# Kernel optimization log

Hardware: AMD Instinct MI355X
Metric: run time of the kernel (lower is better)

The kernel has to match this reference:

```python
import jax, jax.numpy as jnp
import numpy as np

B, S, V, E, HL = 64, 30, 5000, 300, 256
TWOH = 2 * HL
KB, MAPD, MEMD, MLP, NCLS = 512, 512, 512, 1024, 32
L, T, NMOD, NOPS = 8, 9, 9, 6
IH, IW, CIN = 15, 10, 512 + 128


def setup_inputs():
    key = jax.random.key(0)
    ks = iter(jax.random.split(key, 64))
    g = lambda shape, s=0.05: jax.random.normal(next(ks), shape, jnp.float32) * s
    inp = {}
    inp['image'] = g((B, CIN, IH, IW), 1.0)
    inp['ques'] = jax.random.randint(next(ks), (B, S), 0, V)
    ql = jnp.sort(jax.random.randint(next(ks), (B,), 1, S + 1))[::-1]
    inp['q_len'] = ql.at[0].set(S)
    inp['embed_W'] = g((V, E))
    for d in ('f', 'b'):
        inp['lstm_Wi_' + d] = g((E, 4 * HL))
        inp['lstm_Wh_' + d] = g((HL, 4 * HL))
        inp['lstm_b_' + d] = jnp.zeros((4 * HL,), jnp.float32)
    inp['W1'] = g((T, TWOH, TWOH))
    inp['b_1'] = jnp.zeros((TWOH,), jnp.float32)
    inp['W2_w'] = g((2 * TWOH, TWOH)); inp['W2_b'] = jnp.zeros((TWOH,), jnp.float32)
    inp['W3'] = g((TWOH,))
    inp['c_0'] = g((TWOH,), 1.0)
    inp['Wmod'] = g((TWOH, NMOD))
    inp['ic1_w'] = g((KB, CIN)); inp['ic1_b'] = g((KB,), 1.0)
    inp['ic2_w'] = g((KB, KB)); inp['ic2_b'] = g((KB,), 1.0)
    inp['i2m_w'] = g((MAPD, KB)); inp['i2m_b'] = g((MAPD,), 1.0)
    inp['t2m_w'] = g((TWOH, MAPD)); inp['t2m_b'] = jnp.zeros((MAPD,), jnp.float32)
    inp['cell3_ow'] = g((4, NOPS), 1.0)
    inp['cell3_cw'] = g((4, MAPD)); inp['cell3_cb'] = jnp.zeros((4,), jnp.float32)
    inp['cell4_ow'] = g((2, NOPS), 1.0)
    inp['cell4_cw'] = g((2, MAPD)); inp['cell4_cb'] = jnp.zeros((2,), jnp.float32)
    inp['ans_ow'] = g((2, NOPS), 1.0)
    inp['ans_W'] = g((2, 2 * MAPD, MEMD)); inp['ans_b'] = jnp.zeros((2, MEMD), jnp.float32)
    inp['out1_w'] = g((TWOH + MEMD, MLP)); inp['out1_b'] = jnp.zeros((MLP,), jnp.float32)
    inp['out2_w'] = g((MLP, NCLS)); inp['out2_b'] = jnp.zeros((NCLS,), jnp.float32)
    return inp


def _conv1x1(x, w, b):
    return jnp.einsum('bchw,oc->bohw', x, w) + b[None, :, None, None]


def _lstm_dir(xW, Wh, mask, reverse):
    # xW: [S,B,4H], mask: [S,B,1] ; torch LSTM gate order i,f,g,o
    Bn, Hn = xW.shape[1], Wh.shape[0]
    def step(carry, inp):
        h, c = carry
        xw, m = inp
        z = xw + h @ Wh
        i, f, gg, o = jnp.split(z, 4, axis=-1)
        cn = jax.nn.sigmoid(f) * c + jax.nn.sigmoid(i) * jnp.tanh(gg)
        hn = jax.nn.sigmoid(o) * jnp.tanh(cn)
        return (jnp.where(m, hn, h), jnp.where(m, cn, c)), jnp.where(m, hn, 0.0)
    init = (jnp.zeros((Bn, Hn), xW.dtype), jnp.zeros((Bn, Hn), xW.dtype))
    (hF, _), outs = jax.lax.scan(step, init, (xW, mask), reverse=reverse)
    return hF, outs


def _mix3(ow, x, a, t):
    # soft op mixing (DARTS-style) for 3-input cells: x [B,D,H,W], a [B,H,W], t [B,D]
    w = jax.nn.softmax(ow)
    a4 = a[:, None]; t4 = t[:, :, None, None]
    ops = (x * t4, x + t4, x * a4, x * t4 * a4, x, a4 * t4)
    return jax.nn.elu(sum(w[k] * ops[k] for k in range(NOPS)))


def _mix4(ow, x, a1, a2, t):
    w = jax.nn.softmax(ow)
    a14 = a1[:, None]; a24 = a2[:, None]; t4 = t[:, :, None, None]
    ops = (x * t4, x + t4, x * a14, x * a24, x * a14 * a24, x * t4 * (a14 + a24))
    return jax.nn.elu(sum(w[k] * ops[k] for k in range(NOPS)))


def _forward(image, ques, q_len, embed_W, lstm_Wi_f, lstm_Wh_f, lstm_b_f, lstm_Wi_b, lstm_Wh_b, lstm_b_b, W1, b_1, W2_w, W2_b, W3, c_0, Wmod, ic1_w, ic1_b, ic2_w, ic2_b, i2m_w, i2m_b, t2m_w, t2m_b, cell3_ow, cell3_cw, cell3_cb, cell4_ow, cell4_cw, cell4_cb, ans_ow, ans_W, ans_b, out1_w, out1_b, out2_w, out2_b):
    # img_conv (1x1 conv -> ELU -> 1x1 conv)
    x = jax.nn.elu(_conv1x1(image, ic1_w, ic1_b))
    x = _conv1x1(x, ic2_w, ic2_b)
    Bn, _, Hh, Ww = x.shape
    Sn = ques.shape[1]
    # bi-LSTM over the (packed, i.e. masked) question
    emb = embed_W[ques]                                   # [B,S,E]
    mask = (jnp.arange(Sn)[None, :] < q_len[:, None])     # [B,S]
    mT = mask.T[:, :, None].astype(x.dtype) > 0           # [S,B,1] bool
    xWf = (emb @ lstm_Wi_f + lstm_b_f).transpose(1, 0, 2)
    xWb = (emb @ lstm_Wi_b + lstm_b_b).transpose(1, 0, 2)
    hF, oF = _lstm_dir(xWf, lstm_Wh_f, mT, False)
    hB, oB = _lstm_dir(xWb, lstm_Wh_b, mT, True)
    lstm_out = jnp.concatenate([oF, oB], -1).transpose(1, 0, 2)  # [B,S,2H], zero at pads
    q = jnp.concatenate([hF, hB], -1)                            # [B,2H]
    img_map = _conv1x1(x, i2m_w, i2m_b)                          # [B,MAP,H,W]
    stack = jnp.zeros((Bn, Hh, Ww, L), x.dtype)
    p = jnp.zeros((Bn, L), x.dtype).at[:, 0].set(1.0)
    mem = jnp.zeros((Bn, MEMD), x.dtype)
    c_prev = jnp.tile(c_0[None], (Bn, 1))
    e0 = jnp.zeros((L,), x.dtype).at[0].set(1.0)
    imp_loss = jnp.float32(0.0)
    read = lambda st, pp: jnp.einsum('bhwl,bl->bhw', st, pp)
    dec = lambda pp: jnp.concatenate([pp[:, 1:], jnp.zeros_like(pp[:, :1])], 1) + pp * e0
    for t in range(T):
        u = jnp.concatenate([q @ W1[t] + b_1, c_prev], 1) @ W2_w + W2_b  # [B,2H]
        wl = u @ Wmod                                                     # [B,9]
        ls = jax.nn.log_softmax(wl, axis=1)
        imp_loss = imp_loss - jnp.sum(jnp.exp(ls) * ls)
        w = jnp.exp(ls)
        attn = jax.nn.softmax(jnp.einsum('bsh,h->bs', lstm_out * u[:, None, :], W3), axis=1)
        c = jnp.einsum('bs,bsh->bh', attn, lstm_out)
        c_prev = c
        tmap = c @ t2m_w + t2m_b
        stacks, ps = [], []
        a_top = read(stack, p)     # attention at stack top
        # modules 0-3: overwrite at current pointer (pointer shift is commented out in source)
        for m in range(4):
            out = jnp.einsum('bdhw,d->bhw', _mix3(cell3_ow[m], img_map, a_top, tmap), cell3_cw[m]) + cell3_cb[m]
            pb = p[:, None, None, :]
            stacks.append(stack * (1.0 - pb) + out[..., None] * pb)
            ps.append(p)
        # modules 4-5: pop one (soft pointer decrement), then write
        p_dec = dec(p)
        a2 = read(stack, p_dec)
        for m in range(2):
            out = jnp.einsum('bdhw,d->bhw', _mix4(cell4_ow[m], img_map, a_top, a2, tmap), cell4_cw[m]) + cell4_cb[m]
            pb = p_dec[:, None, None, :]
            stacks.append(stack * (1.0 - pb) + out[..., None] * pb)
            ps.append(p_dec)
        # modules 6-7: answer cells -> memory update, stack untouched
        pooled6 = jnp.mean(_mix3(ans_ow[0], img_map, a_top, tmap), axis=(2, 3))
        mem6 = jnp.concatenate([pooled6, tmap], 1) @ ans_W[0] + ans_b[0]
        stacks.append(stack); ps.append(p)
        pooled7 = jnp.mean(_mix4(ans_ow[1], img_map, a_top, a2, tmap), axis=(2, 3))
        mem7 = jnp.concatenate([pooled7, tmap], 1) @ ans_W[1] + ans_b[1]
        stacks.append(stack); ps.append(p_dec)
        # module 8: NoOp
        stacks.append(stack); ps.append(p)
        # soft mixing over modules (the scatter-heavy part)
        stack = jnp.einsum('bm,bmhwl->bhwl', w, jnp.stack(stacks, 1))
        p = jnp.einsum('bm,bml->bl', w, jnp.stack(ps, 1))
        mem = w[:, 6:7] * mem6 + w[:, 7:8] * mem7 + (1.0 - w[:, 6:7] - w[:, 7:8]) * mem
    h1 = jax.nn.elu(jnp.concatenate([q, mem], 1) @ out1_w + out1_b)
    logits = h1 @ out2_w + out2_b
    return logits, imp_loss


def reference(image, ques, q_len, embed_W, lstm_Wi_f, lstm_Wh_f, lstm_b_f, lstm_Wi_b, lstm_Wh_b, lstm_b_b, W1, b_1, W2_w, W2_b, W3, c_0, Wmod, ic1_w, ic1_b, ic2_w, ic2_b, i2m_w, i2m_b, t2m_w, t2m_b, cell3_ow, cell3_cw, cell3_cb, cell4_ow, cell4_cw, cell4_cb, ans_ow, ans_W, ans_b, out1_w, out1_b, out2_w, out2_b):
    return _forward(image, ques, q_len, embed_W, lstm_Wi_f, lstm_Wh_f, lstm_b_f, lstm_Wi_b, lstm_Wh_b, lstm_b_b, W1, b_1, W2_w, W2_b, W3, c_0, Wmod, ic1_w, ic1_b, ic2_w, ic2_b, i2m_w, i2m_b, t2m_w, t2m_b, cell3_ow, cell3_cw, cell3_cb, cell4_ow, cell4_cw, cell4_cb, ans_ow, ans_W, ans_b, out1_w, out1_b, out2_w, out2_b)
```

## Files before the change

kernel.cpp:

```cpp
#include <hip/hip_runtime.h>
#include <hip/hip_fp16.h>
#include <math.h>

#define DEV __device__ __forceinline__

DEV float fexp(float x){ return __expf(x); }
DEV float elu_(float x){ return x > 0.f ? x : fexp(x) - 1.f; }
DEV float sigm_(float x){ return 1.f/(1.f + fexp(-x)); }
DEV float tanh_(float x){ float e = fexp(2.f*x); return 1.f - 2.f/(e + 1.f); }
DEV unsigned bf16r(float x){ unsigned u = __float_as_uint(x);
  return (u + 0x7fffu + ((u>>16)&1u)) >> 16; }
DEV float blo(unsigned u){ return __uint_as_float(u << 16); }
DEV float bhi(unsigned u){ return __uint_as_float(u & 0xffff0000u); }
DEV float bl(unsigned short u){ return __uint_as_float(((unsigned)u) << 16); }

using frag  = __attribute__((ext_vector_type(8))) short;
using fragh = __attribute__((ext_vector_type(8))) _Float16;
using f32x4 = __attribute__((ext_vector_type(4))) float;

DEV uint4 cload16w(const void* p){
  uint4 r;
  asm volatile("global_load_dwordx4 %0, %1, off sc0 sc1\n\ts_waitcnt vmcnt(0)"
               : "=v"(r) : "v"(p) : "memory");
  return r;
// ... 171 lines not shown
    const short* bk = Bbase + (((size_t)kc*Ng) << 9);
    frag b0 = *(const frag*)(bk);
    frag b1 = *(const frag*)(bk + 512);
    frag b2 = *(const frag*)(bk + 1024);
    frag b3 = *(const frag*)(bk + 1536);
    acc0 = __builtin_amdgcn_mfma_f32_16x16x32_bf16(a, b0, acc0, 0, 0, 0);
    acc1 = __builtin_amdgcn_mfma_f32_16x16x32_bf16(a, b1, acc1, 0, 0, 0);
    acc2 = __builtin_amdgcn_mfma_f32_16x16x32_bf16(a, b2, acc2, 0, 0, 0);
    acc3 = __builtin_amdgcn_mfma_f32_16x16x32_bf16(a, b3, acc3, 0, 0, 0);
  }
  {
    int colb = lane & 15, rowb = (lane >> 4)*4;
#pragma unroll
    for (int r = 0; r < 4; ++r) {
      lds[w][rowb+r][ 0+colb] = acc0[r];
      lds[w][rowb+r][16+colb] = acc1[r];
      lds[w][rowb+r][32+colb] = acc2[r];
      lds[w][rowb+r][48+colb] = acc3[r];
    }
  }
  __syncthreads();
  if (mode == 0) {
    float* C = (float*)Cout;
    int mloc = lane >> 2, q4 = lane & 3;
    size_t rowoff = (size_t)(mt*16 + mloc)*N + ncol0 + q4*16;
#pragma unroll
    for (int i = 0; i < 4; ++i) {
      float4 v = *(float4*)&lds[w][mloc][q4*16 + i*4];
      const float* bp = bias + ncol0 + q4*16 + i*4;
      v.x += bp[0]; v.y += bp[1]; v.z += bp[2]; v.w += bp[3];
      if (act) { v.x = elu_(v.x); v.y = elu_(v.y); v.z = elu_(v.z); v.w = elu_(v.w); }
      *(float4*)&C[rowoff + i*4] = v;
    }
  } else if (mode == 1) {
    short* C = (short*)Cout;
    int m = lane & 15, qb = (lane >> 4)*8;
#pragma unroll
    for (int h = 0; h < 2; ++h) {
      int nl = h*32 + qb;
      unsigned o[4];
#pragma unroll
      for (int jj = 0; jj < 4; ++jj) {
        float v0 = lds[w][m][nl + 2*jj]     + bias[ncol0 + nl + 2*jj];
        float v1 = lds[w][m][nl + 2*jj + 1] + bias[ncol0 + nl + 2*jj + 1];
        if (act) { v0 = elu_(v0); v1 = elu_(v1); }
        o[jj] = bf16r(v0) | (bf16r(v1) << 16);
      }
      *(uint4*)(C + (((size_t)mt*KCout + (ncol0 >> 5) + h) << 9) + lane*8)
          = make_uint4(o[0], o[1], o[2], o[3]);
    }
  } else {
    unsigned short* C = (unsigned short*)Cout;
    int row = lane >> 2, cb = (lane & 3)*16;
#pragma unroll
    for (int h = 0; h < 2; ++h) {
      unsigned o[4];
#pragma unroll
      for (int jj = 0; jj < 4; ++jj) {
        float v0 = lds[w][row][cb + h*8 + 2*jj]     + bias[ncol0 + cb + h*8 + 2*jj];
        float v1 = lds[w][row][cb + h*8 + 2*jj + 1] + bias[ncol0 + cb + h*8 + 2*jj + 1];
        if (act) { v0 = elu_(v0); v1 = elu_(v1); }
        o[jj] = bf16r(v0) | (bf16r(v1) << 16);
      }
      *(uint4*)&C[(size_t)(mt*16 + row)*N + ncol0 + cb + h*8]
          = make_uint4(o[0], o[1], o[2], o[3]);
    }
  }
}

__global__ __launch_bounds__(512)
void gemm64b_k(const float* __restrict__ A1, long zA1, int K1log,
               const float* __restrict__ A2, int K2,
               const float* __restrict__ B, long zB,
               const float* __restrict__ bias, int zbias,
               float* __restrict__ C, long zC, int N, int act)
{
  const int K1 = 1 << K1log;
  const int Kt = K1 + K2;
  __shared__ __align__(16) float As[8][1024];
  __shared__ float part[8][8][64];
  const int tid = threadIdx.x;
  const int z = blockIdx.z;
  const int r0 = blockIdx.y*8;
  {
    const float* a1 = A1 + (size_t)z*zA1;
    const int nf4 = (8*K1) >> 2;
    for (int e4 = tid; e4 < nf4; e4 += 512) {
      int r = e4 >> (K1log-2);
      int k4 = (e4 & ((K1>>2)-1)) << 2;
      *(float4*)&As[r][k4] = *(const float4*)&a1[(size_t)(r0+r)*K1 + k4];
    }
    if (K2 > 0) {
      for (int e4 = tid; e4 < 1024; e4 += 512) {
        int r = e4 >> 7;
        int k4 = (e4 & 127) << 2;
        *(float4*)&As[r][K1+k4] = *(const float4*)&A2[(size_t)(r0+r)*512 + k4];
      }
    }
  }
  __syncthreads();
  const int lane = tid & 63, w = tid >> 6;
  const int n = blockIdx.x*64 + lane;
  const bool nv = n < N;
  const int kseg = Kt >> 3;
  const int k0 = w*kseg;
  const float* Bp = B + (size_t)z*zB + (size_t)k0*N + (nv ? n : 0);
  float acc[8] = {0,0,0,0,0,0,0,0};
#pragma unroll 8
  for (int kk = 0; kk < kseg; ++kk) {
    float bv = nv ? Bp[(size_t)kk*N] : 0.f;
    int k = k0 + kk;
#pragma unroll
    for (int r = 0; r < 8; ++r) acc[r] += As[r][k]*bv;
  }
#pragma unroll
  for (int r = 0; r < 8; ++r) part[w][r][lane] = acc[r];
  __syncthreads();
  {
    int r = tid >> 6, c = tid & 63;
    int nn = blockIdx.x*64 + c;
    if (nn < N) {
      float s = 0.f;
#pragma unroll
      for (int w2 = 0; w2 < 8; ++w2) s += part[w2][r][c];
      s += bias ? bias[(size_t)z*zbias + nn] : 0.f;
      if (act == 1) s = elu_(s);
      C[(size_t)z*zC + (size_t)(r0+r)*N + nn] = s;
    }
  }
}

__global__ __launch_bounds__(256)
void lstmc1_k(const float* __restrict__ xWf, const float* __restrict__ xWb,
              const unsigned* __restrict__ whT, const int* __restrict__ qlen,
              unsigned long long* __restrict__ hbuf, int* __restrict__ flags,
              float* __restrict__ lstm_out, float* __restrict__ qout,
              const short* __restrict__ c1Ap, const short* __restrict__ c1Bp,
              const float* __restrict__ c1bias, short* __restrict__ c1out)
{
  const int tid = threadIdx.x, lane = tid & 63, w = tid >> 6;
  __shared__ union {
    unsigned short Wl[65536];
    float lds[4][16][68];
  } sm;

  if (blockIdx.x >= 32) {
    const int bx2 = (int)blockIdx.x - 32;
    const int mt = (bx2 >> 3)*4 + w;
    const int ncol0 = (bx2 & 7)*64;
    const short* Abase = c1Ap + (((size_t)mt*20) << 9) + lane*8;
    const short* Bbase = c1Bp + (((size_t)(bx2 & 7)*4) << 9) + lane*8;
    f32x4 acc0 = {0.f,0.f,0.f,0.f}, acc1 = acc0, acc2 = acc0, acc3 = acc0;
#pragma unroll 2
    for (int kc = 0; kc < 20; ++kc) {
      frag a = *(const frag*)(Abase + ((size_t)kc << 9));
      const short* bk = Bbase + (((size_t)kc*32) << 9);
      frag b0 = *(const frag*)(bk);
      frag b1 = *(const frag*)(bk + 512);
      frag b2 = *(const frag*)(bk + 1024);
      frag b3 = *(const frag*)(bk + 1536);
      acc0 = __builtin_amdgcn_mfma_f32_16x16x32_bf16(a, b0, acc0, 0, 0, 0);
      acc1 = __builtin_amdgcn_mfma_f32_16x16x32_bf16(a, b1, acc1, 0, 0, 0);
      acc2 = __builtin_amdgcn_mfma_f32_16x16x32_bf16(a, b2, acc2, 0, 0, 0);
      acc3 = __builtin_amdgcn_mfma_f32_16x16x32_bf16(a, b3, acc3, 0, 0, 0);
    }
    {
      int colb = lane & 15, rowb = (lane >> 4)*4;
#pragma unroll
      for (int r = 0; r < 4; ++r) {
        sm.lds[w][rowb+r][ 0+colb] = acc0[r];
        sm.lds[w][rowb+r][16+colb] = acc1[r];
        sm.lds[w][rowb+r][32+colb] = acc2[r];
        sm.lds[w][rowb+r][48+colb] = acc3[r];
      }
    }
    __syncthreads();
    {
      int m = lane & 15, qb = (lane >> 4)*8;
#pragma unroll
      for (int h = 0; h < 2; ++h) {
        int nl = h*32 + qb;
        unsigned o[4];
#pragma unroll
        for (int jj = 0; jj < 4; ++jj) {
          float v0 = elu_(sm.lds[w][m][nl + 2*jj]     + c1bias[ncol0 + nl + 2*jj]);
          float v1 = elu_(sm.lds[w][m][nl + 2*jj + 1] + c1bias[ncol0 + nl + 2*jj + 1]);
          o[jj] = bf16r(v0) | (bf16r(v1) << 16);
        }
        *(uint4*)(c1out + (((size_t)mt*16 + (ncol0 >> 5) + h) << 9) + lane*8)
            = make_uint4(o[0], o[1], o[2], o[3]);
      }
    }
    return;
  }

  const int bx = blockIdx.x;
  const int d = bx & 1, g = (bx >> 1) & 3, n = bx >> 3;
  const int q = lane >> 4, cl = lane & 15;

#pragma unroll 4
  for (int rb = 0; rb < 32; ++rb) {
    int lcrow = rb*8 + (tid >> 5);
    int gt = lcrow >> 6, c = lcrow & 63;
    int zc = gt*256 + n*64 + c;
    uint4 v = *(const uint4*)(whT + (((size_t)d*1024 + zc) << 7) + ((tid & 31) << 2));
    int byteoff = (lcrow << 9) + ((((tid & 31) << 4)) ^ ((lcrow & 7) << 4));
    *(uint4*)((char*)sm.Wl + byteoff) = v;
  }

  const float* xW = d ? xWb : xWf;
  const int b   = g*16 + cl;
  const int c4  = w*16 + q*4;
  const int hc4 = n*64 + c4;
  const int len = qlen[b];
  float cst[4] = {0.f,0.f,0.f,0.f}, hst[4] = {0.f,0.f,0.f,0.f};
  int* flg = flags + ((d*4 + g) << 2);
  const int bofs = (cl & 7) << 4;
  __syncthreads();

  for (int ss = 0; ss < 30; ++ss) {
    const int s = d ? (29 - ss) : ss;
    const float* xr = xW + (size_t)b*30720 + (size_t)s*1024 + hc4;
    f32x4 xwv[4];
#pragma unroll
    for (int gt = 0; gt < 4; ++gt) xwv[gt] = *(const f32x4*)(xr + gt*256);

    if (ss > 0) {
      for (;;) {
        uint4 f4 = cload16w(flg);
        if ((int)f4.x >= ss && (int)f4.y >= ss &&
            (int)f4.z >= ss && (int)f4.w >= ss) break;
      }
      __builtin_amdgcn_sched_barrier(0);
    }
    const char* hbr = (const char*)(hbuf + ((size_t)(((ss & 1)*2 + d)*4 + g) << 9))
                    + (cl << 9) + (q << 4);
    union { uint4 u; fragh f; } hv[8];
#pragma unroll
    for (int ks = 0; ks < 8; ++ks) hv[ks].u = cload16nw(hbr + (ks << 6));
    asm volatile("s_waitcnt vmcnt(0)" ::: "memory");
    __builtin_amdgcn_sched_barrier(0);

    f32x4 acc0 = {0.f,0.f,0.f,0.f}, acc1 = acc0, acc2 = acc0, acc3 = acc0;
#pragma unroll
    for (int ks = 0; ks < 8; ++ks) {
      const int kb = ((ks << 6) + (q << 4)) ^ bofs;
      const char* wb = (const char*)sm.Wl + ((w*16 + cl) << 9) + kb;
      fragh a0 = *(const fragh*)(wb);
      fragh a1 = *(const fragh*)(wb + (64 << 9));
      fragh a2 = *(const fragh*)(wb + (128 << 9));
      fragh a3 = *(const fragh*)(wb + (192 << 9));
      acc0 = __builtin_amdgcn_mfma_f32_16x16x32_f16(a0, hv[ks].f, acc0, 0, 0, 0);
      acc1 = __builtin_amdgcn_mfma_f32_16x16x32_f16(a1, hv[ks].f, acc1, 0, 0, 0);
      acc2 = __builtin_amdgcn_mfma_f32_16x16x32_f16(a2, hv[ks].f, acc2, 0, 0, 0);
      acc3 = __builtin_amdgcn_mfma_f32_16x16x32_f16(a3, hv[ks].f, acc3, 0, 0, 0);
    }
    const bool m = s < len;
    f32x4 lo4;
    float hvv[4];
#pragma unroll
    for (int r = 0; r < 4; ++r) {
      float iv = acc0[r] + xwv[0][r];
      float fv = acc1[r] + xwv[1][r];
      float gv = acc2[r] + xwv[2][r];
      float o_ = acc3[r] + xwv[3][r];
      float cn = sigm_(fv)*cst[r] + sigm_(iv)*tanh_(gv);
      float hn = sigm_(o_)*tanh_(cn);
      float hk = m ? hn : hst[r];
      cst[r] = m ? cn : cst[r];
      hst[r] = hk;
      hvv[r] = hk;
      lo4[r] = m ? hn : 0.f;
    }
    unsigned long long* hbw = hbuf + ((size_t)((((ss & 1) ^ 1)*2 + d)*4 + g) << 9);
    union { unsigned long long u; __half2 h2[2]; } hp;
    hp.h2[0] = __floats2half2_rn(hvv[0], hvv[1]);
    hp.h2[1] = __floats2half2_rn(hvv[2], hvv[3]);
    __hip_atomic_store(hbw + cl*64 + (hc4 >> 2), hp.u,
                       __ATOMIC_RELAXED, __HIP_MEMORY_SCOPE_AGENT);
    *(f32x4*)(lstm_out + (((size_t)b*30 + s) << 9) + (d << 8) + hc4) = lo4;
    asm volatile("s_waitcnt vmcnt(0)" ::: "memory");
    __syncthreads();
    if (tid == 0)
      __hip_atomic_store(&flg[n], ss + 1, __ATOMIC_RELAXED, __HIP_MEMORY_SCOPE_AGENT);
  }
  *(f32x4*)(qout + ((size_t)b << 9) + (d << 8) + hc4) =
      f32x4{hst[0], hst[1], hst[2], hst[3]};
}

__global__ __launch_bounds__(1024)
void step_k(const float* __restrict__ u, const float* __restrict__ Wmod,
            const float* __restrict__ lstm_out, const float* __restrict__ W3,
            const unsigned* __restrict__ t2pp, const float* __restrict__ t2mb,
            float* __restrict__ woutAll, float* __restrict__ imp_part,
            float* __restrict__ cprev, float* __restrict__ tmapv_k, int t,
            const float* __restrict__ tmp1n, const unsigned short* __restrict__ w2bp,
            const float* __restrict__ W2b, float* __restrict__ ubuf,
            int* __restrict__ flags2, int do_u,
            const unsigned short* __restrict__ imapB, const float* __restrict__ tmapv_m,
            float* __restrict__ stack, const float* __restrict__ pvecIn,
            float* __restrict__ pvecOut, const float* __restrict__ swb,
            const float* __restrict__ c3w, const float* __restrict__ c3b,
            const float* __restrict__ c4w, const float* __restrict__ c4b,
            const float* __restrict__ wm_m, float* __restrict__ plt, int do_mod)
{
  const int tid = threadIdx.x;
  const int lane = tid & 63, wave = tid >> 6;
  __shared__ union {
    struct {
      float ush[512]; float sC[512]; float cpart[512]; float tpart[4][512];
      float wl[9]; float sc[32], at[32];
    } k;
    struct {
      __align__(16) float As[8][1024]; float part[16][8][64];
    } uu;
    struct {
      float sT[512]; float pv[8], pd[8], wm[9]; float wpart[16][2][512];
    } m;
  } sm;

  if (blockIdx.x < 64) {
    if (t >= 9) return;
    int b = blockIdx.x;
    if (tid < 512) sm.k.ush[tid] = u[b*512 + tid];
    __syncthreads();
    for (int s = wave; s < 30; s += 16) {
      float acc = 0.f;
      const float* lo = lstm_out + ((size_t)b*30 + s)*512;
#pragma unroll
      for (int h = lane; h < 512; h += 64) acc += lo[h]*sm.k.ush[h]*W3[h];
#pragma unroll
      for (int off = 32; off; off >>= 1) acc += __shfl_down(acc, off);
      if (lane == 0) sm.k.sc[s] = acc;
    }
    if (wave < 9) {
      float acc = 0.f;
#pragma unroll
      for (int k = lane; k < 512; k += 64) acc += sm.k.ush[k]*Wmod[k*9+wave];
#pragma unroll
      for (int off = 32; off; off >>= 1) acc += __shfl_down(acc, off);
      if (lane == 0) sm.k.wl[wave] = acc;
    }
    __syncthreads();
    if (tid == 0) {
      float mx = sm.k.wl[0];
      for (int m = 1; m < 9; ++m) mx = fmaxf(mx, sm.k.wl[m]);
      float s = 0.f;
      for (int m = 0; m < 9; ++m) s += fexp(sm.k.wl[m]-mx);
      float ls = logf(s);
      float ent = 0.f;
      for (int m = 0; m < 9; ++m) {
        float l = sm.k.wl[m]-mx-ls;
        float w = fexp(l);
        woutAll[t*576 + b*9 + m] = w;
        ent -= w*l;
      }
      imp_part[t*64+b] = ent;
    }
    if (wave == 1) {
      float v = (lane < 30) ? sm.k.sc[lane] : -3.4e38f;
      float mx = v;
#pragma unroll
      for (int off = 32; off; off >>= 1) mx = fmaxf(mx, __shfl_xor(mx, off));
      float e = (lane < 30) ? fexp(v-mx) : 0.f;
      float ssum = e;
#pragma unroll
      for (int off = 32; off; off >>= 1) ssum += __shfl_xor(ssum, off);
      if (lane < 30) sm.k.at[lane] = e/ssum;
    }
    __syncthreads();
    {
      int h = tid & 511, seg = tid >> 9;
      float acc = 0.f;
      int s0 = seg ? 15 : 0, s1 = seg ? 30 : 15;
      for (int s = s0; s < s1; ++s) acc += sm.k.at[s]*lstm_out[((size_t)b*30 + s)*512 + h];
      if (seg) sm.k.cpart[h] = acc;
      __syncthreads();
      if (!seg) {
        float tot = acc + sm.k.cpart[h];
        cstore4(&cprev[b*512+h], tot);
        sm.k.sC[h] = tot;
      }
    }
    asm volatile("s_waitcnt vmcnt(0)" ::: "memory");
    __syncthreads();
    if (tid == 0)
      __hip_atomic_store(&flags2[b], t + 1, __ATOMIC_RELAXED, __HIP_MEMORY_SCOPE_AGENT);
    {
      int c2 = tid & 255, ks = tid >> 8;
      float a0 = 0.f, a1 = 0.f;
      const unsigned* tp = t2pp + c2;
#pragma unroll 8
      for (int k = ks*128; k < ks*128 + 128; ++k) {
        float cv = sm.k.sC[k];
        unsigned wv2 = tp[(size_t)k*256];
        a0 += cv*blo(wv2);
        a1 += cv*bhi(wv2);
      }
      sm.k.tpart[ks][c2]       = a0;
      sm.k.tpart[ks][256 + c2] = a1;
    }
    __syncthreads();
    if (tid < 512) {
      float v = sm.k.tpart[0][tid] + sm.k.tpart[1][tid]
              + sm.k.tpart[2][tid] + sm.k.tpart[3][tid];
      tmapv_k[b*512 + tid] = v + t2mb[tid];
    }
    return;
  }

  if (blockIdx.x < 128) {
    if (!do_u) return;
    const int x = (int)blockIdx.x - 64;
    const int r0 = (x >> 3) * 8, nc0 = (x & 7) * 64;
    {
      int r = tid >> 7, k4 = (tid & 127) << 2;
      *(float4*)&sm.uu.As[r][k4] = *(const float4*)&tmp1n[(size_t)(r0+r)*512 + k4];
    }
    if (tid == 0) {
      for (;;) {
        uint4 f0 = cload16w(flags2 + r0);
        uint4 f1 = cload16w(flags2 + r0 + 4);
        if ((int)f0.x > t && (int)f0.y > t && (int)f0.z > t && (int)f0.w > t &&
            (int)f1.x > t && (int)f1.y > t && (int)f1.z > t && (int)f1.w > t) break;
      }
    }
    __syncthreads();
    {
      int r = tid >> 7, c4 = (tid & 127) << 2;
      union { uint4 u4; float4 f4; } v;
      v.u4 = cload16nw(&cprev[(size_t)(r0+r)*512 + c4]);
      asm volatile("s_waitcnt vmcnt(0)" ::: "memory");
      *(float4*)&sm.uu.As[r][512 + c4] = v.f4;
    }
    __syncthreads();
    const int k0 = wave * 64;
    const unsigned short* Bp = w2bp + (size_t)k0*512 + nc0 + lane;
    float acc[8] = {0,0,0,0,0,0,0,0};
#pragma unroll 4
    for (int kk = 0; kk < 64; ++kk) {
      float bv = bl(Bp[(size_t)kk*512]);
#pragma unroll
      for (int r = 0; r < 8; ++r) acc[r] += sm.uu.As[r][k0+kk] * bv;
    }
#pragma unroll
    for (int r = 0; r < 8; ++r) sm.uu.part[wave][r][lane] = acc[r];
    __syncthreads();
    if (tid < 512) {
      int r = tid >> 6, c = tid & 63;
      float s2 = 0.f;
#pragma unroll
      for (int w2 = 0; w2 < 16; ++w2) s2 += sm.uu.part[w2][r][c];
      ubuf[(size_t)(r0 + r)*512 + nc0 + c] = s2 + W2b[nc0 + c];
    }
    return;
  }

  if (!do_mod) return;
  const int mb = (int)blockIdx.x - 128;
  const int b = mb & 63, pb = mb >> 6;
  if (tid < 512) sm.m.sT[tid] = tmapv_m[b*512 + tid];
  if (tid >= 512 && tid < 520) sm.m.pv[tid-512] = pvecIn[b*8 + (tid-512)];
  if (tid >= 576 && tid < 585) sm.m.wm[tid-576] = wm_m[b*9 + (tid-576)];
  __syncthreads();
  if (tid < 8) {
    int l = tid;
    sm.m.pd[l] = (l < 7 ? sm.m.pv[l+1] : 0.f) + (l == 0 ? sm.m.pv[0] : 0.f);
  }
  __syncthreads();
  if (pb == 0 && tid < 8) {
    int l = tid;
    float WP = sm.m.wm[0]+sm.m.wm[1]+sm.m.wm[2]+sm.m.wm[3] + sm.m.wm[6] + sm.m.wm[8];
    float WD = sm.m.wm[4]+sm.m.wm[5] + sm.m.wm[7];
    pvecOut[b*8+l] = WP*sm.m.pv[l] + WD*sm.m.pd[l];
  }

  float W[8][6];
#pragma unroll
  for (int m = 0; m < 8; ++m)
#pragma unroll
    for (int i = 0; i < 6; ++i) W[m][i] = swb[m*6+i];
  float W03 = sm.m.wm[0]+sm.m.wm[1]+sm.m.wm[2]+sm.m.wm[3];
  float W45 = sm.m.wm[4]+sm.m.wm[5];

  float acc6[8], acc7[8];
#pragma unroll
  for (int i = 0; i < 8; ++i) { acc6[i] = 0.f; acc7[i] = 0.f; }

  for (int pi = 0; pi < 2; ++pi) {
    int p = pb*32 + wave*2 + pi;
    if (p < 150) {
      const float* st = stack + ((size_t)b*150 + p)*8;
      float a = 0.f, av2 = 0.f;
#pragma unroll
      for (int l = 0; l < 8; ++l) { float v = st[l]; a += v*sm.m.pv[l]; av2 += v*sm.m.pd[l]; }
      float part[6] = {0,0,0,0,0,0};
#pragma unroll 2
      for (int i = 0; i < 8; ++i) {
        int d = i*64 + lane;
        float x = bl(imapB[((size_t)b*150 + p)*512 + d]);
        float t2 = sm.m.sT[d];
#pragma unroll
        for (int m = 0; m < 4; ++m) {
          float c1 = W[m][0]*t2 + W[m][1] + W[m][4] + (W[m][2] + W[m][3]*t2)*a;
          float c0 = W[m][1]*t2 + W[m][5]*t2*a;
          part[m] += elu_(c1*x + c0) * c3w[m*512+d];
        }
#pragma unroll
        for (int m = 0; m < 2; ++m) {
          float c1 = W[4+m][0]*t2 + W[4+m][1] + W[4+m][2]*a + W[4+m][3]*av2
                   + W[4+m][4]*a*av2 + W[4+m][5]*t2*(a+av2);
          part[4+m] += elu_(c1*x + W[4+m][1]*t2) * c4w[m*512+d];
        }
        float c16 = W[6][0]*t2 + W[6][1] + W[6][4] + (W[6][2] + W[6][3]*t2)*a;
        float c06 = W[6][1]*t2 + W[6][5]*t2*a;
        acc6[i] += elu_(c16*x + c06);
        float c17 = W[7][0]*t2 + W[7][1] + W[7][2]*a + W[7][3]*av2
                  + W[7][4]*a*av2 + W[7][5]*t2*(a+av2);
        acc7[i] += elu_(c17*x + W[7][1]*t2);
      }
#pragma unroll
      for (int m = 0; m < 6; ++m) {
#pragma unroll
        for (int off = 32; off; off >>= 1) part[m] += __shfl_down(part[m], off);
        part[m] = __shfl(part[m], 0);
      }
      float r3  = sm.m.wm[0]*(part[0]+c3b[0]) + sm.m.wm[1]*(part[1]+c3b[1])
                + sm.m.wm[2]*(part[2]+c3b[2]) + sm.m.wm[3]*(part[3]+c3b[3]);
      float r45 = sm.m.wm[4]*(part[4]+c4b[0]) + sm.m.wm[5]*(part[5]+c4b[1]);
      if (lane < 8) {
        int l = lane;
        size_t idx = ((size_t)b*150 + p)*8 + l;
        stack[idx] = stack[idx]*(1.f - W03*sm.m.pv[l] - W45*sm.m.pd[l])
                   + sm.m.pv[l]*r3 + sm.m.pd[l]*r45;
      }
    }
  }
#pragma unroll
  for (int i = 0; i < 8; ++i) {
    sm.m.wpart[wave][0][i*64+lane] = acc6[i];
    sm.m.wpart[wave][1][i*64+lane] = acc7[i];
  }
  __syncthreads();
  {
    int which = tid >> 9, d = tid & 511;
    float s = 0.f;
#pragma unroll
    for (int w2 = 0; w2 < 16; ++w2) s += sm.m.wpart[w2][which][d];
    atomicAdd(&plt[(size_t)which*32768 + b*512 + d], s * (1.f/150.f));
  }
}

__global__ __launch_bounds__(512)
void ansall_k(const float* __restrict__ plt, const float* __restrict__ tmapv,
              const unsigned short* __restrict__ answp, const float* __restrict__ ansb,
              float* __restrict__ m67o)
{
  const int z = blockIdx.z;
  const int t = z >> 1, zz = z & 1;
  __shared__ __align__(16) float As[8][1024];
  __shared__ float part[8][8][64];
  const int tid = threadIdx.x;
  const int r0 = blockIdx.y*8;
  const int nc0 = blockIdx.x*64;
  const int lane = tid & 63, w = tid >> 6;

  for (int e4 = tid; e4 < 1024; e4 += 512) {
    int r = e4 >> 7, k4 = (e4 & 127) << 2;
    *(float4*)&As[r][k4]     = *(const float4*)&plt[(size_t)z*32768 + (size_t)(r0+r)*512 + k4];
    *(float4*)&As[r][512+k4] = *(const float4*)&tmapv[(size_t)t*32768 + (size_t)(r0+r)*512 + k4];
  }
  __syncthreads();
  {
    const unsigned short* Bp = answp + (size_t)zz*524288
                             + (size_t)(w*128)*512 + nc0 + lane;
    float acc[8] = {0,0,0,0,0,0,0,0};
    int k0 = w*128;
#pragma unroll 8
    for (int kk = 0; kk < 128; ++kk) {
      float bv = bl(Bp[(size_t)kk*512]);
#pragma unroll
      for (int r = 0; r < 8; ++r) acc[r] += As[r][k0+kk]*bv;
    }
#pragma unroll
    for (int r = 0; r < 8; ++r) part[w][r][lane] = acc[r];
  }
  __syncthreads();
  {
    int r = tid >> 6, c = tid & 63;
    float s = 0.f;
#pragma unroll
    for (int w2 = 0; w2 < 8; ++w2) s += part[w2][r][c];
    m67o[(size_t)z*32768 + (size_t)(r0+r)*512 + nc0 + c] = s + ansb[zz*512 + nc0 + c];
  }
}

__global__ __launch_bounds__(512)
void memfin_k(const float* __restrict__ woutAll, const float* __restrict__ m67t,
              float* __restrict__ memb)
{
  int b = blockIdx.x;
  int tid = threadIdx.x;
  __shared__ float w6s[9], w7s[9], coef[9];
  if (tid < 9)       w6s[tid] = woutAll[tid*576 + b*9 + 6];
  else if (tid < 18) w7s[tid-9] = woutAll[(tid-9)*576 + b*9 + 7];
  __syncthreads();
  if (tid == 0) {
    float c = 1.f;
    for (int t = 8; t >= 0; --t) { coef[t] = c; c *= (1.f - w6s[t] - w7s[t]); }
  }
  __syncthreads();
  float acc = 0.f;
#pragma unroll
  for (int t = 0; t < 9; ++t) {
    float m6 = m67t[(((size_t)t*2 + 0)*64 + b)*512 + tid];
    float m7 = m67t[(((size_t)t*2 + 1)*64 + b)*512 + tid];
    acc += coef[t]*(w6s[t]*m6 + w7s[t]*m7);
  }
  memb[b*512 + tid] = acc;
}

__global__ __launch_bounds__(256)
void imp_k(const float* __restrict__ part, float* __restrict__ out)
{
  int lane = threadIdx.x & 63, wave = threadIdx.x >> 6;
  float acc = 0.f;
  for (int i = threadIdx.x; i < 576; i += 256) acc += part[i];
#pragma unroll
  for (int off = 32; off; off >>= 1) acc += __shfl_down(acc, off);
  __shared__ float red[4];
  if (lane == 0) red[wave] = acc;
  __syncthreads();
  if (threadIdx.x == 0) out[0] = red[0]+red[1]+red[2]+red[3];
}

extern "C" void kernel_launch(void* const* d_in, const int* in_sizes, int n_in,
                              void* d_out, int out_size, void* d_ws, size_t ws_size,
                              hipStream_t stream)
{
  (void)in_sizes; (void)n_in; (void)out_size; (void)ws_size;
  const float* image = (const float*)d_in[0];
  const int*   ques  = (const int*)d_in[1];
  const int*   qlen  = (const int*)d_in[2];
  const float* embedW= (const float*)d_in[3];
  const float* Wi_f  = (const float*)d_in[4];
  const float* Wh_f  = (const float*)d_in[5];
  const float* b_f   = (const float*)d_in[6];
  const float* Wi_b  = (const float*)d_in[7];
  const float* Wh_b  = (const float*)d_in[8];
  const float* b_b   = (const float*)d_in[9];
  const float* W1    = (const float*)d_in[10];
  const float* b1    = (const float*)d_in[11];
  const float* W2w   = (const float*)d_in[12];
  const float* W2b   = (const float*)d_in[13];
  const float* W3    = (const float*)d_in[14];
  const float* c0    = (const float*)d_in[15];
  const float* Wmod  = (const float*)d_in[16];
  const float* ic1w  = (const float*)d_in[17];
  const float* ic1b  = (const float*)d_in[18];
  const float* ic2w  = (const float*)d_in[19];
  const float* ic2b  = (const float*)d_in[20];
  const float* i2mw  = (const float*)d_in[21];
  const float* i2mb  = (const float*)d_in[22];
  const float* t2mw  = (const float*)d_in[23];
  const float* t2mb  = (const float*)d_in[24];
  const float* c3ow  = (const float*)d_in[25];
  const float* c3cw  = (const float*)d_in[26];
  const float* c3cb  = (const float*)d_in[27];
  const float* c4ow  = (const float*)d_in[28];
  const float* c4cw  = (const float*)d_in[29];
  const float* c4cb  = (const float*)d_in[30];
  const float* aow   = (const float*)d_in[31];
  const float* ansW  = (const float*)d_in[32];
  const float* ansb  = (const float*)d_in[33];
  const float* o1w   = (const float*)d_in[34];
  const float* o1b   = (const float*)d_in[35];
  const float* o2w   = (const float*)d_in[36];
  const float* o2b   = (const float*)d_in[37];
  float* out = (float*)d_out;
  float* ws  = (float*)d_ws;

  size_t off = 0;
  auto alloc = [&](size_t n){ float* p = ws + off; off += n; return p; };
  short* imgP  = (short*)alloc(600ull*20*64*8/2);
  short* X1p   = (short*)alloc(600ull*16*64*8/2);
  short* X2p   = (short*)alloc(600ull*16*64*8/2);
  short* w1p   = (short*)alloc(20*32*64*8/2);
  short* w2mp  = (short*)alloc(16*32*64*8/2);
  short* w3mp  = (short*)alloc(16*32*64*8/2);
  short* wifp  = (short*)alloc(10*64*64*8/2);
  short* wibp  = (short*)alloc(10*64*64*8/2);
  short* embp  = (short*)alloc(120ull*10*64*8/2);
  unsigned short* imapB = (unsigned short*)alloc(9600ull*512/2);
  unsigned* t2pp = (unsigned*)alloc(512*256);
  unsigned short* w2bp  = (unsigned short*)alloc(524288/2);
  unsigned short* answp = (unsigned short*)alloc(1048576/2);
  float* xWfb  = alloc(64ull*30*1024);
  float* xWbb  = alloc(64ull*30*1024);
  float* lout  = alloc(64ull*30*512);
  float* qbuf  = alloc(64*512);
  float* stck  = alloc(64*150*8);
  float* pvecA = alloc(64*8);
  float* pvecB = alloc(64*8);
  float* memb  = alloc(64*512);
  float* cprev = alloc(64*512);
  float* tmp1a = alloc(9ull*64*512);
  float* ubuf  = alloc(64*512);
  float* wmwA  = alloc(9*64*9);
  float* impp  = alloc(9*64);
  float* swb   = alloc(48);
  float* pl    = alloc(9ull*2*64*512);
  float* m67t  = alloc(9ull*2*64*512);
  float* tmapv = alloc(9ull*64*512);
  float* h1b   = alloc(64*1024);
  unsigned* whT = (unsigned*)alloc(2ull*1024*128);
  float* hbufW  = alloc(32768);
  int*   flagsI = (int*)alloc(256);
  int*   flags2 = flagsI + 64;

  megapack_k<<<12036, 256, 0, stream>>>(
      c0, c3ow, c4ow, aow, stck, pvecA, memb, cprev, swb, pl,
      Wh_f, Wh_b, whT, hbufW, flagsI,
      ic1w, w1p, ic2w, w2mp, i2mw, w3mp, Wi_f, wifp, Wi_b, wibp,
      image, imgP, embedW, ques, embp, t2mw, t2pp,
      W2w, w2bp, ansW, answp);

  gemmM_k<<<dim3(16,30,2), 256, 0, stream>>>(embp, embp, wifp, wibp, b_f, b_b,
                                             xWfb, xWbb, 10, 64, 1024, 0, 0, 0);

  lstmc1_k<<<1232, 256, 0, stream>>>(xWfb, xWbb, whT, qlen,
                                     (unsigned long long*)hbufW, flagsI,
                                     lout, qbuf,
                                     imgP, w1p, ic1b, X1p);

  gemmM_k<<<dim3(8,150,1), 256, 0, stream>>>(X1p, X1p, w2mp, w2mp, ic2b, ic2b,
                                             X2p, X2p, 16, 32, 512, 1, 0, 16);
  gemmM_k<<<dim3(8,150,1), 256, 0, stream>>>(X2p, X2p, w3mp, w3mp, i2mb, i2mb,
                                             imapB, imapB, 16, 32, 512, 2, 0, 0);

  gemm64b_k<<<dim3(8,8,9), 512, 0, stream>>>(
      qbuf, 0, 9, (const float*)nullptr, 0,
      W1, 262144, b1, 0, tmp1a, 32768, 512, 0);
  gemm64b_k<<<dim3(8,8,1), 512, 0, stream>>>(
      tmp1a, 0, 9, cprev, 512, W2w, 0, W2b, 0, ubuf, 0, 512, 0);

  for (int t = 0; t <= 9; ++t) {
    int tm = t - 1;
    int tmc = (tm < 0) ? 0 : tm;
    float* pvIn  = (tmc & 1) ? pvecB : pvecA;
    float* pvOut = (tmc & 1) ? pvecA : pvecB;
    step_k<<<448, 1024, 0, stream>>>(
        ubuf, Wmod, lout, W3, t2pp, t2mb, wmwA, impp,
        cprev, tmapv + (size_t)(t < 9 ? t : 0)*32768, t,
        tmp1a + (size_t)(t < 8 ? t+1 : 0)*32768, w2bp, W2b, ubuf,
        flags2, (t < 8) ? 1 : 0,
        imapB, tmapv + (size_t)tmc*32768, stck, pvIn, pvOut, swb,
        c3cw, c3cb, c4cw, c4cb,
        wmwA + (size_t)tmc*576, pl + (size_t)tmc*65536,
        (t > 0) ? 1 : 0);
  }

  ansall_k<<<dim3(8,8,18), 512, 0, stream>>>(pl, tmapv, answp, ansb, m67t);

  memfin_k<<<64, 512, 0, stream>>>(wmwA, m67t, memb);
  gemm64b_k<<<dim3(16,8,1), 512, 0, stream>>>(
      qbuf, 0, 9, memb, 512, o1w, 0, o1b, 0, h1b, 0, 1024, 1);
  gemm64b_k<<<dim3(1,8,1), 512, 0, stream>>>(
      h1b, 0, 10, (const float*)nullptr, 0, o2w, 0, o2b, 0, out, 0, 32, 0);
  imp_k<<<1, 256, 0, stream>>>(impp, out + 2048);
}
```

Before: 787.0 us.

## Overlap answer-module GEMMs with later step_k launches and fold imp reduction

Adds 64 extra blocks to each step_k launch that compute the answer-module GEMM for timestep t-2, whose inputs (plt, tmapv) are finished by then. This runs that work alongside the recurrent step instead of in one large ansall_k launch at the end, leaving only the last timestep for ansall_k. The imp_loss reduction moves into memfin_k, which removes one kernel launch. In exchange every step launch gets more blocks and a larger shared-memory union.

After: 784.5 us. About the same (-0.3%).

```diff
diff --git a/kernel.cpp b/kernel.cpp
--- a/kernel.cpp
+++ b/kernel.cpp
@@ -497,7 +497,10 @@
             float* __restrict__ pvecOut, const float* __restrict__ swb,
             const float* __restrict__ c3w, const float* __restrict__ c3b,
             const float* __restrict__ c4w, const float* __restrict__ c4b,
-            const float* __restrict__ wm_m, float* __restrict__ plt, int do_mod)
+            const float* __restrict__ wm_m, float* __restrict__ plt, int do_mod,
+            const float* __restrict__ plt_a, const float* __restrict__ tmapv_a,
+            const unsigned short* __restrict__ answp, const float* __restrict__ ansb,
+            float* __restrict__ m67o_a)
 {
   const int tid = threadIdx.x;
   const int lane = tid & 63, wave = tid >> 6;
@@ -512,6 +515,9 @@
     struct {
       float sT[512]; float pv[8], pd[8], wm[9]; float wpart[16][2][512];
     } m;
+    struct {
+      __align__(16) float As[8][1024]; float part[16][8][64];
+    } a;
   } sm;
 
   if (blockIdx.x < 64) {
@@ -651,107 +657,152 @@
     return;
   }
 
-  if (!do_mod) return;
-  const int mb = (int)blockIdx.x - 128;
-  const int b = mb & 63, pb = mb >> 6;
-  if (tid < 512) sm.m.sT[tid] = tmapv_m[b*512 + tid];
-  if (tid >= 512 && tid < 520) sm.m.pv[tid-512] = pvecIn[b*8 + (tid-512)];
-  if (tid >= 576 && tid < 585) sm.m.wm[tid-576] = wm_m[b*9 + (tid-576)];
-  __syncthreads();
-  if (tid < 8) {
-    int l = tid;
-    sm.m.pd[l] = (l < 7 ? sm.m.pv[l+1] : 0.f) + (l == 0 ? sm.m.pv[0] : 0.f);
-  }
-  __syncthreads();
-  if (pb == 0 && tid < 8) {
-    int l = tid;
-    float WP = sm.m.wm[0]+sm.m.wm[1]+sm.m.wm[2]+sm.m.wm[3] + sm.m.wm[6] + sm.m.wm[8];
-    float WD = sm.m.wm[4]+sm.m.wm[5] + sm.m.wm[7];
-    pvecOut[b*8+l] = WP*sm.m.pv[l] + WD*sm.m.pd[l];
-  }
-
-  float W[8][6];
-#pragma unroll
-  for (int m = 0; m < 8; ++m)
-#pragma unroll
-    for (int i = 0; i < 6; ++i) W[m][i] = swb[m*6+i];
-  float W03 = sm.m.wm[0]+sm.m.wm[1]+sm.m.wm[2]+sm.m.wm[3];
-  float W45 = sm.m.wm[4]+sm.m.wm[5];
-
-  float acc6[8], acc7[8];
-#pragma unroll
-  for (int i = 0; i < 8; ++i) { acc6[i] = 0.f; acc7[i] = 0.f; }
-
-  for (int pi = 0; pi < 2; ++pi) {
-    int p = pb*32 + wave*2 + pi;
-    if (p < 150) {
-      const float* st = stack + ((size_t)b*150 + p)*8;
-      float a = 0.f, av2 = 0.f;
-#pragma unroll
-      for (int l = 0; l < 8; ++l) { float v = st[l]; a += v*sm.m.pv[l]; av2 += v*sm.m.pd[l]; }
-      float part[6] = {0,0,0,0,0,0};
+  if (blockIdx.x < 448) {
+    if (!do_mod) return;
+    const int mb = (int)blockIdx.x - 128;
+    const int b = mb & 63, pb = mb >> 6;
+    if (tid < 512) sm.m.sT[tid] = tmapv_m[b*512 + tid];
+    if (tid >= 512 && tid < 520) sm.m.pv[tid-512] = pvecIn[b*8 + (tid-512)];
+    if (tid >= 576 && tid < 585) sm.m.wm[tid-576] = wm_m[b*9 + (tid-576)];
+    __syncthreads();
+    if (tid < 8) {
+      int l = tid;
+      sm.m.pd[l] = (l < 7 ? sm.m.pv[l+1] : 0.f) + (l == 0 ? sm.m.pv[0] : 0.f);
+    }
+    __syncthreads();
+    if (pb == 0 && tid < 8) {
+      int l = tid;
+      float WP = sm.m.wm[0]+sm.m.wm[1]+sm.m.wm[2]+sm.m.wm[3] + sm.m.wm[6] + sm.m.wm[8];
+      float WD = sm.m.wm[4]+sm.m.wm[5] + sm.m.wm[7];
+      pvecOut[b*8+l] = WP*sm.m.pv[l] + WD*sm.m.pd[l];
+    }
+
+    float W[8][6];
+#pragma unroll
+    for (int m = 0; m < 8; ++m)
+#pragma unroll
+      for (int i = 0; i < 6; ++i) W[m][i] = swb[m*6+i];
+    float W03 = sm.m.wm[0]+sm.m.wm[1]+sm.m.wm[2]+sm.m.wm[3];
+    float W45 = sm.m.wm[4]+sm.m.wm[5];
+
+    float acc6[8], acc7[8];
+#pragma unroll
+    for (int i = 0; i < 8; ++i) { acc6[i] = 0.f; acc7[i] = 0.f; }
+
+    for (int pi = 0; pi < 2; ++pi) {
+      int p = pb*32 + wave*2 + pi;
+      if (p < 150) {
+        const float* st = stack + ((size_t)b*150 + p)*8;
+        float a = 0.f, av2 = 0.f;
+#pragma unroll
+        for (int l = 0; l < 8; ++l) { float v = st[l]; a += v*sm.m.pv[l]; av2 += v*sm.m.pd[l]; }
+        float part[6] = {0,0,0,0,0,0};
 #pragma unroll 2
-      for (int i = 0; i < 8; ++i) {
-        int d = i*64 + lane;
-        float x = bl(imapB[((size_t)b*150 + p)*512 + d]);
-        float t2 = sm.m.sT[d];
-#pragma unroll
-        for (int m = 0; m < 4; ++m) {
-          float c1 = W[m][0]*t2 + W[m][1] + W[m][4] + (W[m][2] + W[m][3]*t2)*a;
-          float c0 = W[m][1]*t2 + W[m][5]*t2*a;
-          part[m] += elu_(c1*x + c0) * c3w[m*512+d];
+        for (int i = 0; i < 8; ++i) {
+          int d = i*64 + lane;
+          float x = bl(imapB[((size_t)b*150 + p)*512 + d]);
+          float t2 = sm.m.sT[d];
+#pragma unroll
+          for (int m = 0; m < 4; ++m) {
+            float c1 = W[m][0]*t2 + W[m][1] + W[m][4] + (W[m][2] + W[m][3]*t2)*a;
+            float c0 = W[m][1]*t2 + W[m][5]*t2*a;
+            part[m] += elu_(c1*x + c0) * c3w[m*512+d];
+          }
+#pragma unroll
+          for (int m = 0; m < 2; ++m) {
+            float c1 = W[4+m][0]*t2 + W[4+m][1] + W[4+m][2]*a + W[4+m][3]*av2
+                     + W[4+m][4]*a*av2 + W[4+m][5]*t2*(a+av2);
+            part[4+m] += elu_(c1*x + W[4+m][1]*t2) * c4w[m*512+d];
+          }
+          float c16 = W[6][0]*t2 + W[6][1] + W[6][4] + (W[6][2] + W[6][3]*t2)*a;
+          float c06 = W[6][1]*t2 + W[6][5]*t2*a;
+          acc6[i] += elu_(c16*x + c06);
+          float c17 = W[7][0]*t2 + W[7][1] + W[7][2]*a + W[7][3]*av2
+                    + W[7][4]*a*av2 + W[7][5]*t2*(a+av2);
+          acc7[i] += elu_(c17*x + W[7][1]*t2);
         }
 #pragma unroll
-        for (int m = 0; m < 2; ++m) {
-          float c1 = W[4+m][0]*t2 + W[4+m][1] + W[4+m][2]*a + W[4+m][3]*av2
-                   + W[4+m][4]*a*av2 + W[4+m][5]*t2*(a+av2);
-          part[4+m] += elu_(c1*x + W[4+m][1]*t2) * c4w[m*512+d];
+        for (int m = 0; m < 6; ++m) {
+#pragma unroll
+          for (int off = 32; off; off >>= 1) part[m] += __shfl_down(part[m], off);
+          part[m] = __shfl(part[m], 0);
         }
-        float c16 = W[6][0]*t2 + W[6][1] + W[6][4] + (W[6][2] + W[6][3]*t2)*a;
-        float c06 = W[6][1]*t2 + W[6][5]*t2*a;
-        acc6[i] += elu_(c16*x + c06);
-        float c17 = W[7][0]*t2 + W[7][1] + W[7][2]*a + W[7][3]*av2
-                  + W[7][4]*a*av2 + W[7][5]*t2*(a+av2);
-        acc7[i] += elu_(c17*x + W[7][1]*t2);
-      }
-#pragma unroll
-      for (int m = 0; m < 6; ++m) {
-#pragma unroll
-        for (int off = 32; off; off >>= 1) part[m] += __shfl_down(part[m], off);
-        part[m] = __shfl(part[m], 0);
-      }
-      float r3  = sm.m.wm[0]*(part[0]+c3b[0]) + sm.m.wm[1]*(part[1]+c3b[1])
-                + sm.m.wm[2]*(part[2]+c3b[2]) + sm.m.wm[3]*(part[3]+c3b[3]);
-      float r45 = sm.m.wm[4]*(part[4]+c4b[0]) + sm.m.wm[5]*(part[5]+c4b[1]);
-      if (lane < 8) {
-        int l = lane;
-        size_t idx = ((size_t)b*150 + p)*8 + l;
-        stack[idx] = stack[idx]*(1.f - W03*sm.m.pv[l] - W45*sm.m.pd[l])
-                   + sm.m.pv[l]*r3 + sm.m.pd[l]*r45;
-      }
-    }
-  }
-#pragma unroll
-  for (int i = 0; i < 8; ++i) {
-    sm.m.wpart[wave][0][i*64+lane] = acc6[i];
-    sm.m.wpart[wave][1][i*64+lane] = acc7[i];
-  }
-  __syncthreads();
+        float r3  = sm.m.wm[0]*(part[0]+c3b[0]) + sm.m.wm[1]*(part[1]+c3b[1])
+                  + sm.m.wm[2]*(part[2]+c3b[2]) + sm.m.wm[3]*(part[3]+c3b[3]);
+        float r45 = sm.m.wm[4]*(part[4]+c4b[0]) + sm.m.wm[5]*(part[5]+c4b[1]);
+        if (lane < 8) {
+          int l = lane;
+          size_t idx = ((size_t)b*150 + p)*8 + l;
+          stack[idx] = stack[idx]*(1.f - W03*sm.m.pv[l] - W45*sm.m.pd[l])
+                     + sm.m.pv[l]*r3 + sm.m.pd[l]*r45;
+        }
+      }
+    }
+#pragma unroll
+    for (int i = 0; i < 8; ++i) {
+      sm.m.wpart[wave][0][i*64+lane] = acc6[i];
+      sm.m.wpart[wave][1][i*64+lane] = acc7[i];
+    }
+    __syncthreads();
+    {
+      int which = tid >> 9, d = tid & 511;
+      float s = 0.f;
+#pragma unroll
+      for (int w2 = 0; w2 < 16; ++w2) s += sm.m.wpart[w2][which][d];
+      atomicAdd(&plt[(size_t)which*32768 + b*512 + d], s * (1.f/150.f));
+    }
+    return;
+  }
+
   {
-    int which = tid >> 9, d = tid & 511;
-    float s = 0.f;
-#pragma unroll
-    for (int w2 = 0; w2 < 16; ++w2) s += sm.m.wpart[w2][which][d];
-    atomicAdd(&plt[(size_t)which*32768 + b*512 + d], s * (1.f/150.f));
+    const int tz = t - 2;
+    if (tz < 0 || tz > 7) return;
+    const int bx2 = (int)blockIdx.x - 448;
+    const int r0 = (bx2 >> 3)*8, nc0 = (bx2 & 7)*64;
+#pragma unroll
+    for (int zz = 0; zz < 2; ++zz) {
+      const int z = tz*2 + zz;
+      for (int e4 = tid; e4 < 2048; e4 += 1024) {
+        int r = e4 >> 8, k4 = (e4 & 255) << 2;
+        float4 v = (k4 < 512)
+            ? *(const float4*)&plt_a[(size_t)z*32768 + (size_t)(r0+r)*512 + k4]
+            : *(const float4*)&tmapv_a[(size_t)tz*32768 + (size_t)(r0+r)*512 + (k4-512)];
+        *(float4*)&sm.a.As[r][k4] = v;
+      }
+      __syncthreads();
+      {
+        const unsigned short* Bp = answp + (size_t)zz*524288
+                                 + (size_t)(wave*64)*512 + nc0 + lane;
+        float acc[8] = {0,0,0,0,0,0,0,0};
+        int k0 = wave*64;
+#pragma unroll 4
+        for (int kk = 0; kk < 64; ++kk) {
+          float bv = bl(Bp[(size_t)kk*512]);
+#pragma unroll
+          for (int r = 0; r < 8; ++r) acc[r] += sm.a.As[r][k0+kk]*bv;
+        }
+#pragma unroll
+        for (int r = 0; r < 8; ++r) sm.a.part[wave][r][lane] = acc[r];
+      }
+      __syncthreads();
+      if (tid < 512) {
+        int r = tid >> 6, c = tid & 63;
+        float s = 0.f;
+#pragma unroll
+        for (int w2 = 0; w2 < 16; ++w2) s += sm.a.part[w2][r][c];
+        m67o_a[(size_t)z*32768 + (size_t)(r0+r)*512 + nc0 + c] = s + ansb[zz*512 + nc0 + c];
+      }
+      __syncthreads();
+    }
   }
 }
 
 __global__ __launch_bounds__(512)
 void ansall_k(const float* __restrict__ plt, const float* __restrict__ tmapv,
               const unsigned short* __restrict__ answp, const float* __restrict__ ansb,
-              float* __restrict__ m67o)
+              float* __restrict__ m67o, int zbase)
 {
-  const int z = blockIdx.z;
+  const int z = blockIdx.z + zbase;
   const int t = z >> 1, zz = z & 1;
   __shared__ __align__(16) float As[8][1024];
   __shared__ float part[8][8][64];
@@ -792,11 +843,13 @@
 
 __global__ __launch_bounds__(512)
 void memfin_k(const float* __restrict__ woutAll, const float* __restrict__ m67t,
-              float* __restrict__ memb)
+              float* __restrict__ memb, const float* __restrict__ impp,
+              float* __restrict__ impout)
 {
   int b = blockIdx.x;
   int tid = threadIdx.x;
   __shared__ float w6s[9], w7s[9], coef[9];
+  __shared__ float red[8];
   if (tid < 9)       w6s[tid] = woutAll[tid*576 + b*9 + 6];
   else if (tid < 18) w7s[tid-9] = woutAll[(tid-9)*576 + b*9 + 7];
   __syncthreads();
@@ -813,20 +866,21 @@
     acc += coef[t]*(w6s[t]*m6 + w7s[t]*m7);
   }
   memb[b*512 + tid] = acc;
-}
-
-__global__ __launch_bounds__(256)
-void imp_k(const float* __restrict__ part, float* __restrict__ out)
-{
-  int lane = threadIdx.x & 63, wave = threadIdx.x >> 6;
-  float acc = 0.f;
-  for (int i = threadIdx.x; i < 576; i += 256) acc += part[i];
-#pragma unroll
-  for (int off = 32; off; off >>= 1) acc += __shfl_down(acc, off);
-  __shared__ float red[4];
-  if (lane == 0) red[wave] = acc;
-  __syncthreads();
-  if (threadIdx.x == 0) out[0] = red[0]+red[1]+red[2]+red[3];
+  if (b == 0) {
+    __syncthreads();
+    int lane = tid & 63, wave = tid >> 6;
+    float a2 = 0.f;
+    for (int i = tid; i < 576; i += 512) a2 += impp[i];
+#pragma unroll
+    for (int off = 32; off; off >>= 1) a2 += __shfl_down(a2, off);
+    if (lane == 0) red[wave] = a2;
+    __syncthreads();
+    if (tid == 0) {
+      float s = 0.f;
+      for (int w2 = 0; w2 < 8; ++w2) s += red[w2];
+      impout[0] = s;
+    }
+  }
 }
 
 extern "C" void kernel_launch(void* const* d_in, const int* in_sizes, int n_in,
@@ -944,7 +998,7 @@
     int tmc = (tm < 0) ? 0 : tm;
     float* pvIn  = (tmc & 1) ? pvecB : pvecA;
     float* pvOut = (tmc & 1) ? pvecA : pvecB;
-    step_k<<<448, 1024, 0, stream>>>(
+    step_k<<<512, 1024, 0, stream>>>(
         ubuf, Wmod, lout, W3, t2pp, t2mb, wmwA, impp,
         cprev, tmapv + (size_t)(t < 9 ? t : 0)*32768, t,
         tmp1a + (size_t)(t < 8 ? t+1 : 0)*32768, w2bp, W2b, ubuf,
@@ -952,15 +1006,15 @@
         imapB, tmapv + (size_t)tmc*32768, stck, pvIn, pvOut, swb,
         c3cw, c3cb, c4cw, c4cb,
         wmwA + (size_t)tmc*576, pl + (size_t)tmc*65536,
-        (t > 0) ? 1 : 0);
-  }
-
-  ansall_k<<<dim3(8,8,18), 512, 0, stream>>>(pl, tmapv, answp, ansb, m67t);
-
-  memfin_k<<<64, 512, 0, stream>>>(wmwA, m67t, memb);
+        (t > 0) ? 1 : 0,
+        pl, tmapv, answp, ansb, m67t);
+  }
+
+  ansall_k<<<dim3(8,8,2), 512, 0, stream>>>(pl, tmapv, answp, ansb, m67t, 16);
+
+  memfin_k<<<64, 512, 0, stream>>>(wmwA, m67t, memb, impp, out + 2048);
   gemm64b_k<<<dim3(16,8,1), 512, 0, stream>>>(
       qbuf, 0, 9, memb, 512, o1w, 0, o1b, 0, h1b, 0, 1024, 1);
   gemm64b_k<<<dim3(1,8,1), 512, 0, stream>>>(
       h1b, 0, 10, (const float*)nullptr, 0, o2w, 0, o2b, 0, out, 0, 32, 0);
-  imp_k<<<1, 256, 0, stream>>>(impp, out + 2048);
-}
+}
```
